# Kernel tuning notes

Measured on AMD Instinct MI355X. Metric: run time of the kernel, lower is better.

## Reference

```python
import jax, jax.numpy as jnp
import numpy as np

B, T, V, S_FIXED, DIM, CV = 4, 256, 1024, 64, 1024, 256


def setup_inputs() -> dict:
    key = jax.random.key(0)
    ks = jax.random.split(key, 8)
    x = jax.random.normal(ks[0], (B, T, DIM), jnp.float32)
    vision = jax.random.normal(ks[1], (B, V, CV), jnp.float32)
    # attention mask (B, V, T): each text token t attends to exactly S_FIXED vision tokens
    scores = jax.random.uniform(ks[2], (B, T, V))
    _, sel = jax.lax.top_k(scores, S_FIXED)  # (B, T, S)
    mask_tv = jnp.zeros((B, T, V), bool)
    mask_tv = mask_tv.at[jnp.arange(B)[:, None, None], jnp.arange(T)[None, :, None], sel].set(True)
    attention_mask = jnp.transpose(mask_tv, (0, 2, 1))  # (B, V, T)
    # xavier-uniform-like params (scale irrelevant for correctness baseline)
    Wu = jax.random.normal(ks[3], (CV, DIM), jnp.float32) * (1.0 / np.sqrt(CV))
    bu = jax.random.normal(ks[4], (DIM,), jnp.float32) * 0.02
    Wk = jax.random.normal(ks[5], (DIM, DIM), jnp.float32) * (1.0 / np.sqrt(DIM))
    Wv = jax.random.normal(ks[6], (DIM, DIM), jnp.float32) * (1.0 / np.sqrt(DIM))
    return {"x": x, "vision": vision, "attention_mask": attention_mask,
            "Wu": Wu, "bu": bu, "Wk": Wk, "Wv": Wv, "S": S_FIXED}


def reference(x, vision, attention_mask, Wu, bu, Wk, Wv, S):
    Bv, Vn, Cv = vision.shape
    Bx, Tn, C = x.shape  # C == dim
    # --- _construct_sparse_inputs ---
    mask_tv = jnp.transpose(attention_mask, (0, 2, 1))  # (B, T, V)
    idx_full = jnp.where(mask_tv, jnp.arange(Vn, dtype=jnp.int32), jnp.int32(Vn))
    # topk(largest=False) == smallest S indices, ascending; pad value = Vn
    index = -jax.lax.top_k(-idx_full, S)[0]  # (B, T, S)
    vision_pad = jnp.concatenate([vision, jnp.zeros((Bv, 1, Cv), vision.dtype)], axis=1)  # (B, V+1, Cv)
    vg = jnp.take_along_axis(vision_pad, index.reshape(Bv, Tn * S, 1), axis=1)
    vg = vg.reshape(Bv, Tn, S, Cv)  # (B, T, S, 256)
    # NOTE: faithful to source — VALID positions receive the -100 bias
    mask_qk = (index != Vn)[..., None].astype(jnp.float32) * (-100.0)  # (B, T, S, 1)
    # --- attention ---
    vu = vg @ Wu + bu           # (B, T, S, dim)
    k = vu @ Wk                 # (B, T, S, dim)
    v = vu @ Wv                 # (B, T, S, dim)
    q = x[:, :, None, :]        # (B, T, 1, dim)
    qk = jnp.einsum('bksc,bktc->bkst', k, q) / jnp.sqrt(jnp.float32(C)) + mask_qk  # (B, T, S, 1)
    sm = jax.nn.softmax(qk.reshape(Bx, -1), axis=-1).reshape(qk.shape)  # softmax over flattened T*S*1
    attn = jnp.einsum('bkst,bksc->bktc', sm, v)  # (B, T, 1, dim)
    return (attn + q).squeeze(2)  # (B, T, dim)
```

## Files before the change

### kernel.cpp

```cpp
#include <hip/hip_runtime.h>
#include <stdint.h>

#define B 4
#define T 256
#define V 1024
#define S 64
#define DIM 1024
#define CV 256

typedef __attribute__((ext_vector_type(8))) short bf16x8;
typedef __attribute__((ext_vector_type(4))) short s16x4;
typedef __attribute__((ext_vector_type(4))) float f32x4;

enum : int {
    WKT_O   = 0,
    WVT_O   = WKT_O + 262144,
    WUB_O   = WVT_O + 262144,
    WKPB_O  = WUB_O + 131072,
    WVPT_O  = WKPB_O + 131072,
    XB_O    = WVPT_O + 131072,
    ZB_O    = XB_O + 262144,
    VB_O    = ZB_O + 131072,
    WB_O    = VB_O + 524288,
    RS_O    = WB_O + 131072,
    PIDX_O  = RS_O + B*T,
    BK_O    = PIDX_O + B*T*S,
    BV_O    = BK_O + DIM,
    BP_O    = BV_O + DIM,
    WS_TOTAL= BP_O + 2*16*1024
};

__device__ __forceinline__ short f2bf(float f) {
    union { float f; unsigned u; } x; x.f = f;
    unsigned r = (x.u + 0x7FFF + ((x.u >> 16) & 1)) >> 16;
    return (short)r;
}
__device__ __forceinline__ float bf2f(short s) {
    union { unsigned u; float f; } x;
    x.u = ((unsigned)(unsigned short)s) << 16;
    return x.f;
}
__device__ __forceinline__ s16x4 cvt4(float4 f) {
    s16x4 o;
    o.x = f2bf(f.x); o.y = f2bf(f.y); o.z = f2bf(f.z); o.w = f2bf(f.w);
    return o;
}

__global__ void stage1(const float* __restrict__ vision, const float* __restrict__ Wu,
                       const float* __restrict__ x, const float* __restrict__ Wk,
                       const float* __restrict__ Wv, const float* __restrict__ bu,
                       const void* __restrict__ maskp,
                       float* __restrict__ ws, int* __restrict__ wsi) {
    __shared__ short tlds[64 * 65];
    __shared__ float tred[4 * 64];
    __shared__ int mc_cnt[16][17];
    __shared__ int sa_flag, sb_flag;
    int blk = blockIdx.x;
    int tid = threadIdx.x;

    if (blk < 2304) {
        const float* src; short* dst; int idx;
        if (blk < 1024)      { src = vision; dst = (short*)(ws + VB_O);  idx = blk; }
        else if (blk < 1280) { src = Wu;     dst = (short*)(ws + WUB_O); idx = blk - 1024; }
        else                 { src = x;      dst = (short*)(ws + XB_O);  idx = blk - 1280; }
        int i = (idx * 256 + tid);
        ((s16x4*)dst)[i] = cvt4(((const float4*)src)[i]);
        return;
    }
    if (blk < 2816) {
        int tile = blk - 2304;
        int which = tile >> 8, t2 = tile & 255;
        int e0 = (t2 >> 4) * 64, d0 = (t2 & 15) * 64;
        const float* src = which ? Wv : Wk;
        short* dst = (short*)(ws + (which ? WVT_O : WKT_O));
        int j = tid & 63, i0 = tid >> 6;
        float pb = 0.f;
#pragma unroll
        for (int p = 0; p < 16; p++) {
            int i = p * 4 + i0;
            float v = src[(size_t)(e0 + i) * DIM + d0 + j];
            tlds[j * 65 + i] = f2bf(v);
            pb += bu[e0 + i] * v;
        }
        tred[i0 * 64 + j] = pb;
        __syncthreads();
#pragma unroll
        for (int p = 0; p < 16; p++) {
            int dd = p * 4 + i0;
            dst[(size_t)(d0 + dd) * DIM + e0 + j] = tlds[dd * 65 + j];
        }
        if (i0 == 0) {
            float s = tred[j] + tred[64 + j] + tred[128 + j] + tred[192 + j];
            ws[BP_O + (which * 16 + (e0 >> 6)) * 1024 + d0 + j] = s;
        }
        return;
    }
    {
        int a = 0, bfl = 0;
        const uchar4* m4 = (const uchar4*)maskp;
#pragma unroll
        for (int jj = 0; jj < 4; jj++) {
            uchar4 u = m4[tid * 4 + jj];
            if (u.y | u.z | u.w) a = 1;
            if (u.x == 0x3f || u.y == 0x3f || u.z == 0x3f || u.w == 0x3f) bfl = 1;
        }
        if (tid == 0) { sa_flag = 0; sb_flag = 0; }
        __syncthreads();
        if (a) sa_flag = 1;
        if (bfl) sb_flag = 1;
        __syncthreads();
    }
    bool byteMode = sa_flag && !sb_flag;
    int mb = blk - 2816;
    int b = mb >> 4, tg = mb & 15;
    int tl = tid & 15, c = tid >> 4;
    int t = tg * 16 + tl;
    int v0 = c * 64;
    unsigned long long bits = 0ull;
    if (byteMode) {
        const uint8_t* m = (const uint8_t*)maskp + (size_t)(b * V + v0) * T + t;
#pragma unroll 8
        for (int j = 0; j < 64; j++)
            if (m[(size_t)j * T] != 0) bits |= 1ull << j;
    } else {
        const int* m = (const int*)maskp + (size_t)(b * V + v0) * T + t;
#pragma unroll 8
        for (int j = 0; j < 64; j++)
            if (m[(size_t)j * T] != 0) bits |= 1ull << j;
    }
    mc_cnt[tl][c] = __popcll(bits);
    __syncthreads();
    int off = 0, total = 0;
#pragma unroll
    for (int cc = 0; cc < 16; cc++) {
        int cn = mc_cnt[tl][cc];
        if (cc < c) off += cn;
        total += cn;
    }
    int base = PIDX_O + (b * T + t) * S;
    while (bits) {
        int j = __ffsll(bits) - 1;
        bits &= bits - 1;
        if (off < S) wsi[base + off] = v0 + j;
        off++;
    }
    if (c == 15)
        for (int j = (total < S ? total : S); j < S; j++) wsi[base + j] = 0;
}

template<int K, int LDA, int LDB>
__device__ __forceinline__ void wave_mma(const short* __restrict__ A0,
                                         const short* __restrict__ B0,
                                         f32x4 acc[2][2]) {
    int lane = threadIdx.x & 63;
    int rw = lane & 15, q = lane >> 4;
    const short* ap0 = A0 + rw * LDA + q * 8;
    const short* ap1 = ap0 + 16 * LDA;
    const short* bp0 = B0 + rw * LDB + q * 8;
    const short* bp1 = bp0 + 16 * LDB;
#pragma unroll 4
    for (int kc = 0; kc < K; kc += 32) {
        bf16x8 a0 = *(const bf16x8*)(ap0 + kc);
        bf16x8 a1 = *(const bf16x8*)(ap1 + kc);
        bf16x8 b0 = *(const bf16x8*)(bp0 + kc);
        bf16x8 b1 = *(const bf16x8*)(bp1 + kc);
        acc[0][0] = __builtin_amdgcn_mfma_f32_16x16x32_bf16(a0, b0, acc[0][0], 0, 0, 0);
        acc[0][1] = __builtin_amdgcn_mfma_f32_16x16x32_bf16(a0, b1, acc[0][1], 0, 0, 0);
        acc[1][0] = __builtin_amdgcn_mfma_f32_16x16x32_bf16(a1, b0, acc[1][0], 0, 0, 0);
        acc[1][1] = __builtin_amdgcn_mfma_f32_16x16x32_bf16(a1, b1, acc[1][1], 0, 0, 0);
    }
}

__global__ void g_prep_mfma(float* __restrict__ ws) {
    if (blockIdx.x >= 128) {
        int which = blockIdx.x - 128;
#pragma unroll
        for (int cch = 0; cch < 4; cch++) {
            int d = cch * 256 + threadIdx.x;
            float s = 0.f;
#pragma unroll
            for (int g = 0; g < 16; g++)
                s += ws[BP_O + (which * 16 + g) * 1024 + d];
            ws[(which ? BV_O : BK_O) + d] = s;
        }
        return;
    }
    int w = blockIdx.x * 4 + (threadIdx.x >> 6);
    int which = w >> 8, rem = w & 255;
    int m0 = (rem >> 5) * 32, n0 = (rem & 31) * 32;
    const short* A = (const short*)(ws + WUB_O) + (size_t)m0 * DIM;
    const short* Bt = (const short*)(ws + (which ? WVT_O : WKT_O)) + (size_t)n0 * DIM;
    f32x4 acc[2][2] = {};
    wave_mma<DIM, DIM, DIM>(A, Bt, acc);
    int lane = threadIdx.x & 63, col = lane & 15, q = lane >> 4;
    if (which == 0) {
        short* o = (short*)(ws + WKPB_O);
#pragma unroll
        for (int i = 0; i < 2; i++)
#pragma unroll
            for (int j = 0; j < 2; j++)
#pragma unroll
                for (int r = 0; r < 4; r++)
                    o[(size_t)(m0 + i * 16 + q * 4 + r) * DIM + n0 + j * 16 + col] =
                        f2bf(acc[i][j][r]);
    } else {
        short* o = (short*)(ws + WVPT_O);
#pragma unroll
        for (int i = 0; i < 2; i++)
#pragma unroll
            for (int j = 0; j < 2; j++) {
                s16x4 v;
                v.x = f2bf(acc[i][j][0]); v.y = f2bf(acc[i][j][1]);
                v.z = f2bf(acc[i][j][2]); v.w = f2bf(acc[i][j][3]);
                *(s16x4*)&o[(size_t)(n0 + j * 16 + col) * CV + m0 + i * 16 + q * 4] = v;
            }
    }
}

__global__ void g_z_mfma(float* __restrict__ ws) {
    int w = blockIdx.x * 4 + (threadIdx.x >> 6);
    int m0 = (w >> 3) * 32, n0 = (w & 7) * 32;
    const short* A = (const short*)(ws + XB_O) + (size_t)m0 * DIM;
    const short* Bt = (const short*)(ws + WKPB_O) + (size_t)n0 * DIM;
    f32x4 acc[2][2] = {};
    wave_mma<DIM, DIM, DIM>(A, Bt, acc);
    int lane = threadIdx.x & 63, col = lane & 15, q = lane >> 4;
    short* zb = (short*)(ws + ZB_O);
#pragma unroll
    for (int i = 0; i < 2; i++)
#pragma unroll
        for (int j = 0; j < 2; j++)
#pragma unroll
            for (int r = 0; r < 4; r++)
                zb[(size_t)(m0 + i * 16 + q * 4 + r) * CV + n0 + j * 16 + col] =
                    f2bf(acc[i][j][r]);
}

__global__ void g_attn(const float* __restrict__ x, float* __restrict__ ws,
                       int* __restrict__ wsi) {
    __shared__ int s_idx[4][64];
    __shared__ float s_ps[4][64];
    int tid = threadIdx.x;
    int lane = tid & 63, wv = tid >> 6;
    int bt = blockIdx.x * 4 + wv, b = bt >> 8;
    s_idx[wv][lane] = wsi[PIDX_O + bt * S + lane];
    float c0p = 0.f;
    const float4* xr = (const float4*)(x + (size_t)bt * DIM);
    const float4* bkr = (const float4*)(ws + BK_O);
#pragma unroll
    for (int j = 0; j < 4; j++) {
        float4 a = xr[lane + 64 * j], k4 = bkr[lane + 64 * j];
        c0p += a.x * k4.x + a.y * k4.y + a.z * k4.z + a.w * k4.w;
    }
    for (int o = 32; o > 0; o >>= 1) c0p += __shfl_xor(c0p, o);
    float c0 = c0p;
    int rw = lane & 15, q = lane >> 4;
    const short* vb = (const short*)(ws + VB_O) + (size_t)b * V * CV;
    const short* zp = (const short*)(ws + ZB_O) + (size_t)bt * CV + q * 8;
    f32x4 acc[4] = {};
#pragma unroll
    for (int mt = 0; mt < 4; mt++) {
        const short* ap = vb + (size_t)s_idx[wv][mt * 16 + rw] * CV + q * 8;
        f32x4 a4 = {0.f, 0.f, 0.f, 0.f};
#pragma unroll
        for (int kc = 0; kc < CV; kc += 32) {
            bf16x8 av = *(const bf16x8*)(ap + kc);
            bf16x8 bv = *(const bf16x8*)(zp + kc);
            a4 = __builtin_amdgcn_mfma_f32_16x16x32_bf16(av, bv, a4, 0, 0, 0);
        }
        acc[mt] = a4;
    }
    if (rw == 0) {
#pragma unroll
        for (int mt = 0; mt < 4; mt++)
#pragma unroll
            for (int r = 0; r < 4; r++)
                s_ps[wv][mt * 16 + q * 4 + r] = acc[mt][r];
    }
    float p = expf((s_ps[wv][lane] + c0) * 0.03125f);
    float rs = p;
    for (int o = 32; o > 0; o >>= 1) rs += __shfl_xor(rs, o);
    s_ps[wv][lane] = p;
    if (lane == 0) ws[RS_O + bt] = rs;
    float4 wa = {0.f, 0.f, 0.f, 0.f};
#pragma unroll 8
    for (int s = 0; s < S; s++) {
        float pv = s_ps[wv][s];
        s16x4 r4 = *(const s16x4*)(vb + (size_t)s_idx[wv][s] * CV + lane * 4);
        wa.x += pv * bf2f(r4.x); wa.y += pv * bf2f(r4.y);
        wa.z += pv * bf2f(r4.z); wa.w += pv * bf2f(r4.w);
    }
    s16x4 o;
    o.x = f2bf(wa.x); o.y = f2bf(wa.y); o.z = f2bf(wa.z); o.w = f2bf(wa.w);
    ((s16x4*)((short*)(ws + WB_O) + (size_t)bt * CV))[lane] = o;
}

__global__ void g_out_mfma(const float* __restrict__ x, float* __restrict__ ws,
                           float* __restrict__ out) {
    int w = blockIdx.x * 4 + (threadIdx.x >> 6);
    int m0 = (w >> 5) * 32, n0 = (w & 31) * 32;
    int lane = threadIdx.x & 63;
    int b = m0 >> 8;
    float4 r4 = *(const float4*)(ws + RS_O + b * 256 + lane * 4);
    float dn = r4.x + r4.y + r4.z + r4.w;
    for (int o = 32; o > 0; o >>= 1) dn += __shfl_xor(dn, o);
    float inv = 1.0f / dn;
    const short* A = (const short*)(ws + WB_O) + (size_t)m0 * CV;
    const short* Bt = (const short*)(ws + WVPT_O) + (size_t)n0 * CV;
    f32x4 acc[2][2] = {};
    wave_mma<CV, CV, CV>(A, Bt, acc);
    int col = lane & 15, q = lane >> 4;
#pragma unroll
    for (int i = 0; i < 2; i++)
#pragma unroll
        for (int r = 0; r < 4; r++) {
            int row = m0 + i * 16 + q * 4 + r;
            float rs = ws[RS_O + row];
#pragma unroll
            for (int j = 0; j < 2; j++) {
                int cc = n0 + j * 16 + col;
                out[(size_t)row * DIM + cc] =
                    x[(size_t)row * DIM + cc] +
                    (acc[i][j][r] + rs * ws[BV_O + cc]) * inv;
            }
        }
}

extern "C" void kernel_launch(void* const* d_in, const int* in_sizes, int n_in,
                              void* d_out, int out_size, void* d_ws, size_t ws_size,
                              hipStream_t stream) {
    (void)in_sizes; (void)n_in; (void)out_size; (void)ws_size;
    const float* x      = (const float*)d_in[0];
    const float* vision = (const float*)d_in[1];
    const void*  mask   = d_in[2];
    const float* Wu     = (const float*)d_in[3];
    const float* bu     = (const float*)d_in[4];
    const float* Wk     = (const float*)d_in[5];
    const float* Wv     = (const float*)d_in[6];
    float* out = (float*)d_out;
    float* ws  = (float*)d_ws;
    int*   wsi = (int*)d_ws;

    stage1<<<2880, 256, 0, stream>>>(vision, Wu, x, Wk, Wv, bu, mask, ws, wsi);
    g_prep_mfma<<<130, 256, 0, stream>>>(ws);
    g_z_mfma<<<64, 256, 0, stream>>>(ws);
    g_attn<<<256, 256, 0, stream>>>(x, ws, wsi);
    g_out_mfma<<<256, 256, 0, stream>>>(x, ws, out);
}
```

Before: 140.6 us.

## Split-K across waves and split attention work to raise block counts

```diff
diff --git a/kernel.cpp b/kernel.cpp
--- a/kernel.cpp
+++ b/kernel.cpp
@@ -171,9 +171,35 @@
     }
 }
 
+__device__ __forceinline__ bool splitk_reduce(f32x4 acc[2][2],
+                                              float (*red)[64][17],
+                                              int wv, int lane) {
+    if (wv > 0) {
+#pragma unroll
+        for (int i = 0; i < 2; i++)
+#pragma unroll
+            for (int j = 0; j < 2; j++)
+#pragma unroll
+                for (int r = 0; r < 4; r++)
+                    red[wv - 1][lane][(i * 2 + j) * 4 + r] = acc[i][j][r];
+    }
+    __syncthreads();
+    if (wv != 0) return false;
+#pragma unroll
+    for (int i = 0; i < 2; i++)
+#pragma unroll
+        for (int j = 0; j < 2; j++)
+#pragma unroll
+            for (int r = 0; r < 4; r++) {
+                int c = (i * 2 + j) * 4 + r;
+                acc[i][j][r] += red[0][lane][c] + red[1][lane][c] + red[2][lane][c];
+            }
+    return true;
+}
+
 __global__ void g_prep_mfma(float* __restrict__ ws) {
-    if (blockIdx.x >= 128) {
-        int which = blockIdx.x - 128;
+    if (blockIdx.x >= 512) {
+        int which = blockIdx.x - 512;
 #pragma unroll
         for (int cch = 0; cch < 4; cch++) {
             int d = cch * 256 + threadIdx.x;
@@ -185,14 +211,17 @@
         }
         return;
     }
-    int w = blockIdx.x * 4 + (threadIdx.x >> 6);
-    int which = w >> 8, rem = w & 255;
+    __shared__ float red[3][64][17];
+    int tile = blockIdx.x;
+    int which = tile >> 8, rem = tile & 255;
     int m0 = (rem >> 5) * 32, n0 = (rem & 31) * 32;
-    const short* A = (const short*)(ws + WUB_O) + (size_t)m0 * DIM;
-    const short* Bt = (const short*)(ws + (which ? WVT_O : WKT_O)) + (size_t)n0 * DIM;
+    int wv = threadIdx.x >> 6, lane = threadIdx.x & 63;
+    const short* A = (const short*)(ws + WUB_O) + (size_t)m0 * DIM + wv * 256;
+    const short* Bt = (const short*)(ws + (which ? WVT_O : WKT_O)) + (size_t)n0 * DIM + wv * 256;
     f32x4 acc[2][2] = {};
-    wave_mma<DIM, DIM, DIM>(A, Bt, acc);
-    int lane = threadIdx.x & 63, col = lane & 15, q = lane >> 4;
+    wave_mma<256, DIM, DIM>(A, Bt, acc);
+    if (!splitk_reduce(acc, red, wv, lane)) return;
+    int col = lane & 15, q = lane >> 4;
     if (which == 0) {
         short* o = (short*)(ws + WKPB_O);
 #pragma unroll
@@ -218,13 +247,16 @@
 }
 
 __global__ void g_z_mfma(float* __restrict__ ws) {
-    int w = blockIdx.x * 4 + (threadIdx.x >> 6);
+    __shared__ float red[3][64][17];
+    int w = blockIdx.x;
     int m0 = (w >> 3) * 32, n0 = (w & 7) * 32;
-    const short* A = (const short*)(ws + XB_O) + (size_t)m0 * DIM;
-    const short* Bt = (const short*)(ws + WKPB_O) + (size_t)n0 * DIM;
+    int wv = threadIdx.x >> 6, lane = threadIdx.x & 63;
+    const short* A = (const short*)(ws + XB_O) + (size_t)m0 * DIM + wv * 256;
+    const short* Bt = (const short*)(ws + WKPB_O) + (size_t)n0 * DIM + wv * 256;
     f32x4 acc[2][2] = {};
-    wave_mma<DIM, DIM, DIM>(A, Bt, acc);
-    int lane = threadIdx.x & 63, col = lane & 15, q = lane >> 4;
+    wave_mma<256, DIM, DIM>(A, Bt, acc);
+    if (!splitk_reduce(acc, red, wv, lane)) return;
+    int col = lane & 15, q = lane >> 4;
     short* zb = (short*)(ws + ZB_O);
 #pragma unroll
     for (int i = 0; i < 2; i++)
@@ -238,29 +270,35 @@
 
 __global__ void g_attn(const float* __restrict__ x, float* __restrict__ ws,
                        int* __restrict__ wsi) {
-    __shared__ int s_idx[4][64];
-    __shared__ float s_ps[4][64];
+    __shared__ int   s_idx[2][64];
+    __shared__ float s_sc[2][64];
+    __shared__ float s_c0[2][2];
+    __shared__ float s_p[2][64];
+    __shared__ float s_wa[2][64][5];
     int tid = threadIdx.x;
     int lane = tid & 63, wv = tid >> 6;
-    int bt = blockIdx.x * 4 + wv, b = bt >> 8;
-    s_idx[wv][lane] = wsi[PIDX_O + bt * S + lane];
+    int pair = wv >> 1, h = wv & 1;
+    int bt = blockIdx.x * 2 + pair, b = bt >> 8;
+    if (h == 0) s_idx[pair][lane] = wsi[PIDX_O + bt * S + lane];
     float c0p = 0.f;
     const float4* xr = (const float4*)(x + (size_t)bt * DIM);
     const float4* bkr = (const float4*)(ws + BK_O);
 #pragma unroll
-    for (int j = 0; j < 4; j++) {
-        float4 a = xr[lane + 64 * j], k4 = bkr[lane + 64 * j];
+    for (int j = 0; j < 2; j++) {
+        int jj = h * 2 + j;
+        float4 a = xr[lane + 64 * jj], k4 = bkr[lane + 64 * jj];
         c0p += a.x * k4.x + a.y * k4.y + a.z * k4.z + a.w * k4.w;
     }
     for (int o = 32; o > 0; o >>= 1) c0p += __shfl_xor(c0p, o);
-    float c0 = c0p;
+    if (lane == 0) s_c0[pair][h] = c0p;
+    __syncthreads();
     int rw = lane & 15, q = lane >> 4;
     const short* vb = (const short*)(ws + VB_O) + (size_t)b * V * CV;
     const short* zp = (const short*)(ws + ZB_O) + (size_t)bt * CV + q * 8;
-    f32x4 acc[4] = {};
-#pragma unroll
-    for (int mt = 0; mt < 4; mt++) {
-        const short* ap = vb + (size_t)s_idx[wv][mt * 16 + rw] * CV + q * 8;
+#pragma unroll
+    for (int mi = 0; mi < 2; mi++) {
+        int mt = h * 2 + mi;
+        const short* ap = vb + (size_t)s_idx[pair][mt * 16 + rw] * CV + q * 8;
         f32x4 a4 = {0.f, 0.f, 0.f, 0.f};
 #pragma unroll
         for (int kc = 0; kc < CV; kc += 32) {
@@ -268,61 +306,78 @@
             bf16x8 bv = *(const bf16x8*)(zp + kc);
             a4 = __builtin_amdgcn_mfma_f32_16x16x32_bf16(av, bv, a4, 0, 0, 0);
         }
-        acc[mt] = a4;
-    }
-    if (rw == 0) {
-#pragma unroll
-        for (int mt = 0; mt < 4; mt++)
+        if (rw == 0) {
 #pragma unroll
             for (int r = 0; r < 4; r++)
-                s_ps[wv][mt * 16 + q * 4 + r] = acc[mt][r];
-    }
-    float p = expf((s_ps[wv][lane] + c0) * 0.03125f);
+                s_sc[pair][mt * 16 + q * 4 + r] = a4[r];
+        }
+    }
+    __syncthreads();
+    float c0 = s_c0[pair][0] + s_c0[pair][1];
+    float p = expf((s_sc[pair][lane] + c0) * 0.03125f);
     float rs = p;
     for (int o = 32; o > 0; o >>= 1) rs += __shfl_xor(rs, o);
-    s_ps[wv][lane] = p;
-    if (lane == 0) ws[RS_O + bt] = rs;
+    s_p[pair][lane] = p;
+    if (h == 0 && lane == 0) ws[RS_O + bt] = rs;
     float4 wa = {0.f, 0.f, 0.f, 0.f};
 #pragma unroll 8
-    for (int s = 0; s < S; s++) {
-        float pv = s_ps[wv][s];
-        s16x4 r4 = *(const s16x4*)(vb + (size_t)s_idx[wv][s] * CV + lane * 4);
+    for (int si = 0; si < 32; si++) {
+        int s = h * 32 + si;
+        float pv = s_p[pair][s];
+        s16x4 r4 = *(const s16x4*)(vb + (size_t)s_idx[pair][s] * CV + lane * 4);
         wa.x += pv * bf2f(r4.x); wa.y += pv * bf2f(r4.y);
         wa.z += pv * bf2f(r4.z); wa.w += pv * bf2f(r4.w);
     }
-    s16x4 o;
-    o.x = f2bf(wa.x); o.y = f2bf(wa.y); o.z = f2bf(wa.z); o.w = f2bf(wa.w);
-    ((s16x4*)((short*)(ws + WB_O) + (size_t)bt * CV))[lane] = o;
+    if (h == 1) {
+        s_wa[pair][lane][0] = wa.x; s_wa[pair][lane][1] = wa.y;
+        s_wa[pair][lane][2] = wa.z; s_wa[pair][lane][3] = wa.w;
+    }
+    __syncthreads();
+    if (h == 0) {
+        wa.x += s_wa[pair][lane][0]; wa.y += s_wa[pair][lane][1];
+        wa.z += s_wa[pair][lane][2]; wa.w += s_wa[pair][lane][3];
+        s16x4 o;
+        o.x = f2bf(wa.x); o.y = f2bf(wa.y); o.z = f2bf(wa.z); o.w = f2bf(wa.w);
+        ((s16x4*)((short*)(ws + WB_O) + (size_t)bt * CV))[lane] = o;
+    }
 }
 
 __global__ void g_out_mfma(const float* __restrict__ x, float* __restrict__ ws,
                            float* __restrict__ out) {
     int w = blockIdx.x * 4 + (threadIdx.x >> 6);
-    int m0 = (w >> 5) * 32, n0 = (w & 31) * 32;
+    int m0 = (w >> 6) * 32, n0 = (w & 63) * 16;
     int lane = threadIdx.x & 63;
     int b = m0 >> 8;
     float4 r4 = *(const float4*)(ws + RS_O + b * 256 + lane * 4);
     float dn = r4.x + r4.y + r4.z + r4.w;
     for (int o = 32; o > 0; o >>= 1) dn += __shfl_xor(dn, o);
     float inv = 1.0f / dn;
-    const short* A = (const short*)(ws + WB_O) + (size_t)m0 * CV;
+    int rw = lane & 15, q = lane >> 4;
+    const short* A  = (const short*)(ws + WB_O)   + (size_t)m0 * CV;
     const short* Bt = (const short*)(ws + WVPT_O) + (size_t)n0 * CV;
-    f32x4 acc[2][2] = {};
-    wave_mma<CV, CV, CV>(A, Bt, acc);
-    int col = lane & 15, q = lane >> 4;
+    const short* ap0 = A + rw * CV + q * 8;
+    const short* ap1 = ap0 + 16 * CV;
+    const short* bp0 = Bt + rw * CV + q * 8;
+    f32x4 acc[2] = {};
+#pragma unroll 4
+    for (int kc = 0; kc < CV; kc += 32) {
+        bf16x8 a0 = *(const bf16x8*)(ap0 + kc);
+        bf16x8 a1 = *(const bf16x8*)(ap1 + kc);
+        bf16x8 b0 = *(const bf16x8*)(bp0 + kc);
+        acc[0] = __builtin_amdgcn_mfma_f32_16x16x32_bf16(a0, b0, acc[0], 0, 0, 0);
+        acc[1] = __builtin_amdgcn_mfma_f32_16x16x32_bf16(a1, b0, acc[1], 0, 0, 0);
+    }
+    int col = lane & 15;
 #pragma unroll
     for (int i = 0; i < 2; i++)
 #pragma unroll
         for (int r = 0; r < 4; r++) {
             int row = m0 + i * 16 + q * 4 + r;
             float rs = ws[RS_O + row];
-#pragma unroll
-            for (int j = 0; j < 2; j++) {
-                int cc = n0 + j * 16 + col;
-                out[(size_t)row * DIM + cc] =
-                    x[(size_t)row * DIM + cc] +
-                    (acc[i][j][r] + rs * ws[BV_O + cc]) * inv;
-            }
+            int cc = n0 + col;
+            out[(size_t)row * DIM + cc] =
+                x[(size_t)row * DIM + cc] +
+                (acc[i][r] + rs * ws[BV_O + cc]) * inv;
         }
 }
 
@@ -342,8 +397,8 @@
     int*   wsi = (int*)d_ws;
 
     stage1<<<2880, 256, 0, stream>>>(vision, Wu, x, Wk, Wv, bu, mask, ws, wsi);
-    g_prep_mfma<<<130, 256, 0, stream>>>(ws);
-    g_z_mfma<<<64, 256, 0, stream>>>(ws);
-    g_attn<<<256, 256, 0, stream>>>(x, ws, wsi);
-    g_out_mfma<<<256, 256, 0, stream>>>(x, ws, out);
-}
+    g_prep_mfma<<<514, 256, 0, stream>>>(ws);
+    g_z_mfma<<<256, 256, 0, stream>>>(ws);
+    g_attn<<<512, 256, 0, stream>>>(x, ws, wsi);
+    g_out_mfma<<<512, 256, 0, stream>>>(x, ws, out);
+}
```

Measured after the change: 115.7 us. -17.7%, faster.
